# Performance work log

Measured on AMD Instinct MI355X. Metric: run time of the kernel, lower is better.

The kernel has to match this reference:

```python
import jax, jax.numpy as jnp
import numpy as np

MAX_DISP = 200


def conv2d(x, w, b):
    # x: [N,C,H,W], w: [O,I,3,3], stride 1, pad 1 == SAME
    y = jax.lax.conv_general_dilated(x, w, (1, 1), 'SAME',
                                     dimension_numbers=('NCHW', 'OIHW', 'NCHW'))
    return y + b[None, :, None, None]


def bn(x, g, b, m, v):
    # eval-mode BatchNorm2d with running stats (eps=1e-5)
    inv = jax.lax.rsqrt(v[None, :, None, None] + 1e-5)
    return g[None, :, None, None] * (x - m[None, :, None, None]) * inv + b[None, :, None, None]


def cost_volume(left, right, max_disp):
    # left, right: [c,h,w]. cost[d,y,x] = sum_c left[c,y,x] * padded[c,y,x+d]
    # where padded = [zeros(c,h,D), right] along w -- exact math of the torch loop.
    c, h, w = left.shape
    padded = jnp.concatenate([jnp.zeros((c, h, max_disp), left.dtype), right], axis=-1)

    def corr(d):
        win = jax.lax.dynamic_slice_in_dim(padded, d, w, axis=2)  # [c,h,w]
        return jnp.sum(left * win, axis=0)  # [h,w]

    return jax.vmap(corr)(jnp.arange(max_disp))  # [D,h,w]


def setup_inputs() -> dict:
    key = jax.random.key(0)
    ks = jax.random.split(key, 32)
    C, H, W = 32, 128, 256
    D = MAX_DISP
    inp = {}
    inp['left'] = jax.random.normal(ks[0], (1, C, H, W), jnp.float32)
    inp['right'] = jax.random.normal(ks[1], (1, C, H, W), jnp.float32)
    chans = [(64, D), (32, 64), (8, 32)]
    i = 2
    for idx, (co, ci) in enumerate(chans, 1):
        inp[f'w{idx}'] = jax.random.normal(ks[i], (co, ci, 3, 3), jnp.float32) * 0.05; i += 1
        inp[f'b{idx}'] = jax.random.normal(ks[i], (co,), jnp.float32) * 0.05; i += 1
        inp[f'g{idx}'] = 1.0 + 0.1 * jax.random.normal(ks[i], (co,), jnp.float32); i += 1
        inp[f'be{idx}'] = 0.1 * jax.random.normal(ks[i], (co,), jnp.float32); i += 1
        inp[f'm{idx}'] = 0.1 * jax.random.normal(ks[i], (co,), jnp.float32); i += 1
        inp[f'v{idx}'] = jax.random.uniform(ks[i], (co,), jnp.float32, minval=0.5, maxval=1.5); i += 1
    inp['w4'] = jax.random.normal(ks[i], (1, 8, 3, 3), jnp.float32) * 0.05; i += 1
    inp['b4'] = jax.random.normal(ks[i], (1,), jnp.float32) * 0.05
    return inp


def reference(left, right, w1, b1, g1, be1, m1, v1, w2, b2, g2, be2, m2, v2,
              w3, b3, g3, be3, m3, v3, w4, b4):
    vol = cost_volume(left[0], right[0], MAX_DISP)[None]  # [1, D, H, W]
    x = jax.nn.relu(bn(conv2d(vol, w1, b1), g1, be1, m1, v1))
    x = jax.nn.relu(bn(conv2d(x, w2, b2), g2, be2, m2, v2))
    x = jax.nn.relu(bn(conv2d(x, w3, b3), g3, be3, m3, v3))
    x = conv2d(x, w4, b4)
    return x[0]  # [1, H, W] (torch squeezes batch dim 0)
```

## Files before the change

### kernel.cpp

```cpp
#include <hip/hip_runtime.h>

#define HH 128
#define WW 256
#define CV_C 32
#define DISP 200

typedef __attribute__((ext_vector_type(4))) float f32x4;
typedef __attribute__((ext_vector_type(8))) short bf16x8;

__device__ inline unsigned short f2bf(float f) {
  unsigned int u = __float_as_uint(f);
  u = (u + 0x7FFFu + ((u >> 16) & 1u)) >> 16;
  return (unsigned short)u;
}

__device__ inline float bf2f(short s) {
  return __uint_as_float(((unsigned int)(unsigned short)s) << 16);
}

#define MAP_YX4()                                   \
  const int slot = bid >> 3;                        \
  const int y = ((bid & 7) << 4) + (slot & 15);     \
  const int x0 = (slot >> 4) << 6;

__global__ __launch_bounds__(256) void k1_cv_pack(
    const float* __restrict__ left, const float* __restrict__ right,
    const float* __restrict__ w1, const float* __restrict__ w2,
    const float* __restrict__ w3, unsigned short* __restrict__ pw1,
    unsigned short* __restrict__ pb2, unsigned short* __restrict__ pb3,
    unsigned short* __restrict__ cost_t) {
  __shared__ unsigned short r_sh[272][40];
  __shared__ unsigned short l_hi[64][40];
  __shared__ unsigned short l_lo[64][40];
  __shared__ unsigned short c_sh[64][224];
  const int bid = blockIdx.x;
  const int tid = threadIdx.x;

  if (bid >= 512) {
    const int b = bid - 512;
    if (b < 504) {
      const int idx = b * 256 + tid;
      const int j = idx & 7;
      const int n = (idx >> 3) & 63;
      const int kg = (idx >> 9) & 3;
      const int cp = idx >> 11;
      const int pos = cp % 9;
      const int chunk = cp / 9;
      const int ci = chunk * 32 + kg * 8 + j;
      float v = 0.f;
      if (ci < 200) v = w1[(n * 200 + ci) * 9 + pos];
      pw1[idx] = f2bf(v);
    } else if (b < 576) {
      const int idx = (b - 504) * 256 + tid;
      const int j = idx & 7;
      const int n = (idx >> 3) & 31;
      const int kg = (idx >> 8) & 3;
      const int kc = (idx >> 10) & 1;
      const int pos = idx >> 11;
      const int ci = kc * 32 + kg * 8 + j;
      pb2[idx] = f2bf(w2[(n * 64 + ci) * 9 + pos]);
    } else {
      const int idx = (b - 576) * 256 + tid;
      const int j = idx & 7;
      const int n = (idx >> 3) & 15;
      const int kg = (idx >> 7) & 3;
      const int pos = idx >> 9;
      const int ci = kg * 8 + j;
      float v = 0.f;
      if (n < 8) v = w3[(n * 32 + ci) * 9 + pos];
      pb3[idx] = f2bf(v);
    }
    return;
  }

  MAP_YX4();
  const int lane = tid & 63;
  const int wv = tid >> 6;
  const int col = lane & 15;
  const int kg = lane >> 4;

  for (int c = wv; c < CV_C; c += 4) {
    const float v = left[(c * HH + y) * WW + x0 + lane];
    const unsigned short h = f2bf(v);
    l_hi[lane][c] = h;
    l_lo[lane][c] = f2bf(v - bf2f(h));
  }
  for (int c = wv; c < CV_C; c += 4) {
    for (int pq = 0; pq < 320; pq += 64) {
      const int p = pq + lane;
      if (p < 272) {
        const int xp = x0 - 208 + p;
        float v = (xp >= 0) ? right[(c * HH + y) * WW + xp] : 0.f;
        r_sh[p][c] = f2bf(v);
      }
    }
  }
  {
    bf16x8 z = {0, 0, 0, 0, 0, 0, 0, 0};
    bf16x8* cz = (bf16x8*)c_sh;
#pragma unroll
    for (int k = 0; k < 7; ++k) cz[k * 256 + tid] = z;
  }
  __syncthreads();

  const bf16x8 b_hi = *(const bf16x8*)&l_hi[16 * wv + col][kg * 8];
  const bf16x8 b_lo = *(const bf16x8*)&l_lo[16 * wv + col][kg * 8];

  for (int t = 0; t < 14; ++t) {
    const int pq = 16 * (wv - t) + 208;
    const bf16x8 a_r = *(const bf16x8*)&r_sh[pq + col][kg * 8];
    f32x4 acc = {0.f, 0.f, 0.f, 0.f};
    acc = __builtin_amdgcn_mfma_f32_16x16x32_bf16(a_r, b_hi, acc, 0, 0, 0);
    acc = __builtin_amdgcn_mfma_f32_16x16x32_bf16(a_r, b_lo, acc, 0, 0, 0);
#pragma unroll
    for (int r = 0; r < 4; ++r) {
      const int d = 200 - 16 * t + kg * 4 + r - col;
      if (d >= 0 && d < DISP) c_sh[16 * wv + col][d] = f2bf(acc[r]);
    }
  }
  __syncthreads();

#pragma unroll
  for (int k = 0; k < 7; ++k) {
    const int s = k * 256 + tid;
    const int x = s / 28;
    const int dv = s - x * 28;
    *reinterpret_cast<bf16x8*>(&cost_t[(y * WW + x0 + x) * 224 + dv * 8]) =
        *reinterpret_cast<const bf16x8*>(&c_sh[x][dv * 8]);
  }
}

__global__ __launch_bounds__(256) void conv1_mfma_kernel(
    const unsigned short* __restrict__ cost_t,
    const unsigned short* __restrict__ pw,
    const float* __restrict__ bias, const float* __restrict__ gam,
    const float* __restrict__ bet, const float* __restrict__ mean,
    const float* __restrict__ var, unsigned short* __restrict__ out_t) {
  __shared__ unsigned short a_sh[4 * 66 * 40];
  __shared__ unsigned short b_sh[9 * 4 * 64 * 8];
  const int bid = blockIdx.x;
  const int tid = threadIdx.x;
  const int slot = bid >> 3;
  const int p = ((bid & 7) << 3) + (slot & 7);
  const int y0 = p << 1;
  const int x0 = (slot >> 3) << 6;
  const int lane = tid & 63;
  const int wv = tid >> 6;
  const int r = wv >> 1;
  const int n0 = (wv & 1) * 32;
  const int col = lane & 15;
  const int kg = lane >> 4;

  long goff[5];
  int laddr[5];
  bool gvalid[5], lvalid[5];
#pragma unroll
  for (int it = 0; it < 5; ++it) {
    const int i = tid + it * 256;
    lvalid[it] = i < 1056;
    const int row = i / 264;
    const int rem = i % 264;
    const int xx = rem >> 2;
    const int q = rem & 3;
    const int gy = y0 + row - 1;
    const int gx = x0 - 1 + xx;
    gvalid[it] = lvalid[it] && gy >= 0 && gy < HH && gx >= 0 && gx < WW;
    goff[it] = gvalid[it] ? (long)(gy * WW + gx) * 224 + q * 8 : 0;
    laddr[it] = (row * 66 + xx) * 40 + q * 8;
  }

  f32x4 acc[4][2];
#pragma unroll
  for (int i = 0; i < 4; ++i)
#pragma unroll
    for (int jx = 0; jx < 2; ++jx) acc[i][jx] = 0.f;

  const bf16x8* pwv = (const bf16x8*)pw;
  bf16x8* bsl = (bf16x8*)b_sh;
  const bf16x8 zero = {0, 0, 0, 0, 0, 0, 0, 0};
  bf16x8 stgA[5], stgB[9];

#pragma unroll
  for (int it = 0; it < 5; ++it)
    stgA[it] = gvalid[it] ? *reinterpret_cast<const bf16x8*>(&cost_t[goff[it]])
                          : zero;
#pragma unroll
  for (int it = 0; it < 9; ++it) stgB[it] = pwv[tid + it * 256];
#pragma unroll
  for (int it = 0; it < 5; ++it)
    if (lvalid[it]) *reinterpret_cast<bf16x8*>(&a_sh[laddr[it]]) = stgA[it];
#pragma unroll
  for (int it = 0; it < 9; ++it) bsl[tid + it * 256] = stgB[it];
  __syncthreads();

  for (int chunk = 0; chunk < 7; ++chunk) {
    if (chunk < 6) {
#pragma unroll
      for (int it = 0; it < 5; ++it)
        stgA[it] = gvalid[it] ? *reinterpret_cast<const bf16x8*>(
                                    &cost_t[goff[it] + (chunk + 1) * 32])
                              : zero;
      const bf16x8* pwn = pwv + (chunk + 1) * 2304;
#pragma unroll
      for (int it = 0; it < 9; ++it) stgB[it] = pwn[tid + it * 256];
    }
    const bf16x8* av = (const bf16x8*)a_sh;
#pragma unroll
    for (int pos = 0; pos < 9; ++pos) {
      const int ky = pos / 3;
      const int kx = pos % 3;
      const bf16x8 b0v = bsl[(pos * 4 + kg) * 64 + n0 + col];
      const bf16x8 b1v = bsl[(pos * 4 + kg) * 64 + n0 + 16 + col];
      bf16x8 af[4];
#pragma unroll
      for (int mt = 0; mt < 4; ++mt)
        af[mt] = av[((r + ky) * 66 + mt * 16 + col + kx) * 5 + kg];
#pragma unroll
      for (int mt = 0; mt < 4; ++mt) {
        acc[mt][0] =
            __builtin_amdgcn_mfma_f32_16x16x32_bf16(af[mt], b0v, acc[mt][0], 0, 0, 0);
        acc[mt][1] =
            __builtin_amdgcn_mfma_f32_16x16x32_bf16(af[mt], b1v, acc[mt][1], 0, 0, 0);
      }
    }
    if (chunk < 6) {
      __syncthreads();
#pragma unroll
      for (int it = 0; it < 5; ++it)
        if (lvalid[it]) *reinterpret_cast<bf16x8*>(&a_sh[laddr[it]]) = stgA[it];
#pragma unroll
      for (int it = 0; it < 9; ++it) bsl[tid + it * 256] = stgB[it];
      __syncthreads();
    }
  }

  const int y = y0 + r;
#pragma unroll
  for (int nf = 0; nf < 2; ++nf) {
    const int c = n0 + nf * 16 + col;
    const float inv = rsqrtf(var[c] + 1e-5f);
    const float sc = gam[c] * inv;
    const float sh = bet[c] - mean[c] * sc;
    const float bb = bias[c];
#pragma unroll
    for (int mt = 0; mt < 4; ++mt) {
#pragma unroll
      for (int rr = 0; rr < 4; ++rr) {
        const int m = mt * 16 + kg * 4 + rr;
        float vv = (acc[mt][nf][rr] + bb) * sc + sh;
        vv = fmaxf(vv, 0.f);
        out_t[((y * WW + x0 + m) << 6) + c] = f2bf(vv);
      }
    }
  }
}

__global__ __launch_bounds__(256) void conv2_mfma_kernel(
    const unsigned short* __restrict__ in_t,
    const unsigned short* __restrict__ pb,
    const float* __restrict__ bias, const float* __restrict__ gam,
    const float* __restrict__ bet, const float* __restrict__ mean,
    const float* __restrict__ var, unsigned short* __restrict__ out_t) {
  __shared__ unsigned short a_sh[3 * 66 * 64];
  __shared__ unsigned short b_sh[18432];
  char* const ab = (char*)a_sh;
  const int bid = blockIdx.x;
  const int tid = threadIdx.x;
  MAP_YX4();
  const int lane = tid & 63;
  const int wv = tid >> 6;
  const int m0 = (wv >> 1) * 32;
  const int n0 = (wv & 1) * 16;
  const int col = lane & 15;
  const int kg = lane >> 4;

  f32x4 acc[2];
  acc[0] = 0.f;
  acc[1] = 0.f;

  {
    const bf16x8* pbv = (const bf16x8*)pb;
    bf16x8* bsl = (bf16x8*)b_sh;
#pragma unroll
    for (int it = 0; it < 9; ++it) bsl[tid + it * 256] = pbv[tid + it * 256];
  }
  for (int i = tid; i < 1584; i += 256) {
    const int r = i >> 3;
    const int q = i & 7;
    const int rowy = r / 66;
    const int xx = r % 66;
    const int gy = y + rowy - 1;
    const int gx = x0 - 1 + xx;
    bf16x8 v = {0, 0, 0, 0, 0, 0, 0, 0};
    if (gy >= 0 && gy < HH && gx >= 0 && gx < WW)
      v = *reinterpret_cast<const bf16x8*>(&in_t[((gy * WW + gx) << 6) + q * 8]);
    const int byte = ((r << 7) + (q << 4)) ^ ((r & 7) << 4);
    *reinterpret_cast<bf16x8*>(ab + byte) = v;
  }
  __syncthreads();

  const bf16x8* bsl = (const bf16x8*)b_sh;
#pragma unroll
  for (int pos = 0; pos < 9; ++pos) {
    const int ky = pos / 3;
    const int kx = pos % 3;
#pragma unroll
    for (int kc = 0; kc < 2; ++kc) {
      const bf16x8 bv = bsl[((pos * 2 + kc) * 4 + kg) * 32 + n0 + col];
#pragma unroll
      for (int mf = 0; mf < 2; ++mf) {
        const int r = ky * 66 + m0 + mf * 16 + col + kx;
        const int byte = ((r << 7) + (kc << 6) + (kg << 4)) ^ ((r & 7) << 4);
        const bf16x8 av = *reinterpret_cast<const bf16x8*>(ab + byte);
        acc[mf] = __builtin_amdgcn_mfma_f32_16x16x32_bf16(av, bv, acc[mf], 0, 0, 0);
      }
    }
  }

  const int c = n0 + col;
  const float inv = rsqrtf(var[c] + 1e-5f);
  const float sc = gam[c] * inv;
  const float sh = bet[c] - mean[c] * sc;
  const float bb = bias[c];
#pragma unroll
  for (int mf = 0; mf < 2; ++mf) {
#pragma unroll
    for (int rr = 0; rr < 4; ++rr) {
      const int m = m0 + mf * 16 + kg * 4 + rr;
      float vv = (acc[mf][rr] + bb) * sc + sh;
      vv = fmaxf(vv, 0.f);
      out_t[((y * WW + x0 + m) << 5) + c] = f2bf(vv);
    }
  }
}

__global__ __launch_bounds__(256) void conv3_mfma_kernel(
    const unsigned short* __restrict__ in_t,
    const unsigned short* __restrict__ pb,
    const float* __restrict__ bias, const float* __restrict__ gam,
    const float* __restrict__ bet, const float* __restrict__ mean,
    const float* __restrict__ var, unsigned short* __restrict__ out_t) {
  __shared__ unsigned short a_sh[3 * 66 * 32];
  __shared__ unsigned short b_sh[4608];
  char* const ab = (char*)a_sh;
  const int bid = blockIdx.x;
  const int tid = threadIdx.x;
  MAP_YX4();
  const int lane = tid & 63;
  const int wv = tid >> 6;
  const int m0 = wv * 16;
  const int col = lane & 15;
  const int kg = lane >> 4;

  f32x4 acc = 0.f;

  {
    const bf16x8* pbv = (const bf16x8*)pb;
    bf16x8* bsl = (bf16x8*)b_sh;
    for (int s = tid; s < 576; s += 256) bsl[s] = pbv[s];
  }
  for (int i = tid; i < 792; i += 256) {
    const int r = i >> 2;
    const int q = i & 3;
    const int rowy = r / 66;
    const int xx = r % 66;
    const int gy = y + rowy - 1;
    const int gx = x0 - 1 + xx;
    bf16x8 v = {0, 0, 0, 0, 0, 0, 0, 0};
    if (gy >= 0 && gy < HH && gx >= 0 && gx < WW)
      v = *reinterpret_cast<const bf16x8*>(&in_t[((gy * WW + gx) << 5) + q * 8]);
    const int byte = ((r << 6) + (q << 4)) ^ ((r & 3) << 4);
    *reinterpret_cast<bf16x8*>(ab + byte) = v;
  }
  __syncthreads();

  const bf16x8* bsl = (const bf16x8*)b_sh;
#pragma unroll
  for (int pos = 0; pos < 9; ++pos) {
    const int ky = pos / 3;
    const int kx = pos % 3;
    const bf16x8 bv = bsl[(pos * 4 + kg) * 16 + col];
    const int r = ky * 66 + m0 + col + kx;
    const int byte = ((r << 6) + (kg << 4)) ^ ((r & 3) << 4);
    const bf16x8 av = *reinterpret_cast<const bf16x8*>(ab + byte);
    acc = __builtin_amdgcn_mfma_f32_16x16x32_bf16(av, bv, acc, 0, 0, 0);
  }

  if (col < 8) {
    const int c = col;
    const float inv = rsqrtf(var[c] + 1e-5f);
    const float sc = gam[c] * inv;
    const float sh = bet[c] - mean[c] * sc;
    const float bb = bias[c];
#pragma unroll
    for (int rr = 0; rr < 4; ++rr) {
      const int m = m0 + kg * 4 + rr;
      float vv = (acc[rr] + bb) * sc + sh;
      vv = fmaxf(vv, 0.f);
      out_t[((y * WW + x0 + m) << 3) + c] = f2bf(vv);
    }
  }
}

__global__ __launch_bounds__(256) void conv4_kernel(
    const unsigned short* __restrict__ in_t, const float* __restrict__ w4,
    const float* __restrict__ b4, float* __restrict__ out) {
  const int bid = blockIdx.x;
  const int y = ((bid & 7) << 4) + (bid >> 3);
  const int x = threadIdx.x;

  float wr[3][3][8];
#pragma unroll
  for (int ci = 0; ci < 8; ++ci)
#pragma unroll
    for (int ky = 0; ky < 3; ++ky)
#pragma unroll
      for (int kx = 0; kx < 3; ++kx) wr[ky][kx][ci] = w4[(ci * 3 + ky) * 3 + kx];

  float acc = b4[0];
#pragma unroll
  for (int ky = 0; ky < 3; ++ky) {
    const int gy = y + ky - 1;
    if (gy < 0 || gy >= HH) continue;
#pragma unroll
    for (int kx = 0; kx < 3; ++kx) {
      const int gx = x + kx - 1;
      if (gx < 0 || gx >= WW) continue;
      const bf16x8 v =
          *reinterpret_cast<const bf16x8*>(&in_t[((gy << 8) + gx) << 3]);
#pragma unroll
      for (int ci = 0; ci < 8; ++ci) acc += bf2f(v[ci]) * wr[ky][kx][ci];
    }
  }
  out[y * WW + x] = acc;
}

extern "C" void kernel_launch(void* const* d_in, const int* in_sizes, int n_in,
                              void* d_out, int out_size, void* d_ws,
                              size_t ws_size, hipStream_t stream) {
  const float* left = (const float*)d_in[0];
  const float* right = (const float*)d_in[1];
  const float* w1 = (const float*)d_in[2];
  const float* b1 = (const float*)d_in[3];
  const float* g1 = (const float*)d_in[4];
  const float* be1 = (const float*)d_in[5];
  const float* m1 = (const float*)d_in[6];
  const float* v1 = (const float*)d_in[7];
  const float* w2 = (const float*)d_in[8];
  const float* b2 = (const float*)d_in[9];
  const float* g2 = (const float*)d_in[10];
  const float* be2 = (const float*)d_in[11];
  const float* m2 = (const float*)d_in[12];
  const float* v2 = (const float*)d_in[13];
  const float* w3 = (const float*)d_in[14];
  const float* b3 = (const float*)d_in[15];
  const float* g3 = (const float*)d_in[16];
  const float* be3 = (const float*)d_in[17];
  const float* m3 = (const float*)d_in[18];
  const float* v3 = (const float*)d_in[19];
  const float* w4 = (const float*)d_in[20];
  const float* b4 = (const float*)d_in[21];

  char* ws = (char*)d_ws;
  unsigned short* cost_t = (unsigned short*)ws;
  char* region = ws + 14680064;
  unsigned short* pw1 = (unsigned short*)(region + 0);
  unsigned short* pb2 = (unsigned short*)(region + 262144);
  unsigned short* pb3 = (unsigned short*)(region + 327680);
  unsigned short* o1t = (unsigned short*)(region + 393216);
  unsigned short* o2t = (unsigned short*)(region + 4587520);
  unsigned short* o3t = (unsigned short*)(region + 6684672);
  float* o4 = (float*)d_out;

  k1_cv_pack<<<1106, 256, 0, stream>>>(left, right, w1, w2, w3, pw1, pb2, pb3,
                                       cost_t);
  conv1_mfma_kernel<<<256, 256, 0, stream>>>(cost_t, pw1, b1, g1, be1, m1, v1,
                                             o1t);
  conv2_mfma_kernel<<<512, 256, 0, stream>>>(o1t, pb2, b2, g2, be2, m2, v2,
                                             o2t);
  conv3_mfma_kernel<<<512, 256, 0, stream>>>(o2t, pb3, b3, g3, be3, m3, v3,
                                             o3t);
  conv4_kernel<<<128, 256, 0, stream>>>(o3t, w4, b4, o4);
}
```

Baseline: 48.88 us.

## Fuse conv3 and conv4 into one kernel with halo recompute in LDS

```diff
diff --git a/kernel.cpp b/kernel.cpp
--- a/kernel.cpp
+++ b/kernel.cpp
@@ -334,38 +334,41 @@
   }
 }
 
-__global__ __launch_bounds__(256) void conv3_mfma_kernel(
+__global__ __launch_bounds__(256) void conv34_fused_kernel(
     const unsigned short* __restrict__ in_t,
     const unsigned short* __restrict__ pb,
     const float* __restrict__ bias, const float* __restrict__ gam,
     const float* __restrict__ bet, const float* __restrict__ mean,
-    const float* __restrict__ var, unsigned short* __restrict__ out_t) {
-  __shared__ unsigned short a_sh[3 * 66 * 32];
+    const float* __restrict__ var, const float* __restrict__ w4,
+    const float* __restrict__ b4, float* __restrict__ out) {
+  __shared__ unsigned short o2s[5 * 84 * 32];
   __shared__ unsigned short b_sh[4608];
-  char* const ab = (char*)a_sh;
+  __shared__ unsigned short o3s[3 * 80 * 8];
+  char* const ab = (char*)o2s;
   const int bid = blockIdx.x;
   const int tid = threadIdx.x;
   MAP_YX4();
   const int lane = tid & 63;
   const int wv = tid >> 6;
-  const int m0 = wv * 16;
   const int col = lane & 15;
   const int kg = lane >> 4;
-
-  f32x4 acc = 0.f;
 
   {
     const bf16x8* pbv = (const bf16x8*)pb;
     bf16x8* bsl = (bf16x8*)b_sh;
     for (int s = tid; s < 576; s += 256) bsl[s] = pbv[s];
   }
-  for (int i = tid; i < 792; i += 256) {
+  if (tid < 240) {
+    bf16x8 z = {0, 0, 0, 0, 0, 0, 0, 0};
+    ((bf16x8*)o3s)[tid] = z;
+  }
+  for (int i = tid; i < 1680; i += 256) {
     const int r = i >> 2;
     const int q = i & 3;
-    const int rowy = r / 66;
-    const int xx = r % 66;
-    const int gy = y + rowy - 1;
-    const int gx = x0 - 1 + xx;
+    const int rowy = r / 84;
+    const int xx = r % 84;
+    const int gy = y - 2 + rowy;
+    const int gx = x0 - 2 + xx;
     bf16x8 v = {0, 0, 0, 0, 0, 0, 0, 0};
     if (gy >= 0 && gy < HH && gx >= 0 && gx < WW)
       v = *reinterpret_cast<const bf16x8*>(&in_t[((gy * WW + gx) << 5) + q * 8]);
@@ -375,64 +378,65 @@
   __syncthreads();
 
   const bf16x8* bsl = (const bf16x8*)b_sh;
-#pragma unroll
-  for (int pos = 0; pos < 9; ++pos) {
-    const int ky = pos / 3;
-    const int kx = pos % 3;
-    const bf16x8 bv = bsl[(pos * 4 + kg) * 16 + col];
-    const int r = ky * 66 + m0 + col + kx;
-    const int byte = ((r << 6) + (kg << 4)) ^ ((r & 3) << 4);
-    const bf16x8 av = *reinterpret_cast<const bf16x8*>(ab + byte);
-    acc = __builtin_amdgcn_mfma_f32_16x16x32_bf16(av, bv, acc, 0, 0, 0);
-  }
-
-  if (col < 8) {
-    const int c = col;
-    const float inv = rsqrtf(var[c] + 1e-5f);
-    const float sc = gam[c] * inv;
-    const float sh = bet[c] - mean[c] * sc;
-    const float bb = bias[c];
-#pragma unroll
-    for (int rr = 0; rr < 4; ++rr) {
-      const int m = m0 + kg * 4 + rr;
-      float vv = (acc[rr] + bb) * sc + sh;
-      vv = fmaxf(vv, 0.f);
-      out_t[((y * WW + x0 + m) << 3) + c] = f2bf(vv);
-    }
-  }
-}
-
-__global__ __launch_bounds__(256) void conv4_kernel(
-    const unsigned short* __restrict__ in_t, const float* __restrict__ w4,
-    const float* __restrict__ b4, float* __restrict__ out) {
-  const int bid = blockIdx.x;
-  const int y = ((bid & 7) << 4) + (bid >> 3);
-  const int x = threadIdx.x;
-
-  float wr[3][3][8];
-#pragma unroll
-  for (int ci = 0; ci < 8; ++ci)
-#pragma unroll
-    for (int ky = 0; ky < 3; ++ky)
-#pragma unroll
-      for (int kx = 0; kx < 3; ++kx) wr[ky][kx][ci] = w4[(ci * 3 + ky) * 3 + kx];
-
-  float acc = b4[0];
-#pragma unroll
-  for (int ky = 0; ky < 3; ++ky) {
-    const int gy = y + ky - 1;
-    if (gy < 0 || gy >= HH) continue;
-#pragma unroll
-    for (int kx = 0; kx < 3; ++kx) {
-      const int gx = x + kx - 1;
-      if (gx < 0 || gx >= WW) continue;
-      const bf16x8 v =
-          *reinterpret_cast<const bf16x8*>(&in_t[((gy << 8) + gx) << 3]);
-#pragma unroll
-      for (int ci = 0; ci < 8; ++ci) acc += bf2f(v[ci]) * wr[ky][kx][ci];
-    }
-  }
-  out[y * WW + x] = acc;
+  const int c3 = col < 8 ? col : 7;
+  const float inv3 = rsqrtf(var[c3] + 1e-5f);
+  const float sc3 = gam[c3] * inv3;
+  const float sh3 = bet[c3] - mean[c3] * sc3;
+  const float bb3 = bias[c3];
+
+  for (int jb = wv; jb < 15; jb += 4) {
+    const int ry = jb / 5;
+    const int xt = jb % 5;
+    f32x4 acc = {0.f, 0.f, 0.f, 0.f};
+#pragma unroll
+    for (int pos = 0; pos < 9; ++pos) {
+      const int ky = pos / 3;
+      const int kx = pos % 3;
+      const bf16x8 bv = bsl[(pos * 4 + kg) * 16 + col];
+      const int r = (ry + ky) * 84 + 16 * xt + col + kx;
+      const int byte = ((r << 6) + (kg << 4)) ^ ((r & 3) << 4);
+      const bf16x8 av = *reinterpret_cast<const bf16x8*>(ab + byte);
+      acc = __builtin_amdgcn_mfma_f32_16x16x32_bf16(av, bv, acc, 0, 0, 0);
+    }
+    if (col < 8) {
+      const int gyo = y - 1 + ry;
+#pragma unroll
+      for (int rr = 0; rr < 4; ++rr) {
+        const int pxl = 16 * xt + kg * 4 + rr;
+        const int gxo = x0 - 1 + pxl;
+        if (gyo >= 0 && gyo < HH && gxo >= 0 && gxo < WW) {
+          float vv = (acc[rr] + bb3) * sc3 + sh3;
+          vv = fmaxf(vv, 0.f);
+          o3s[(ry * 80 + pxl) * 8 + col] = f2bf(vv);
+        }
+      }
+    }
+  }
+  __syncthreads();
+
+  if (tid < 64) {
+    const int x = x0 + tid;
+    float wr[3][3][8];
+#pragma unroll
+    for (int ci = 0; ci < 8; ++ci)
+#pragma unroll
+      for (int ky = 0; ky < 3; ++ky)
+#pragma unroll
+        for (int kx = 0; kx < 3; ++kx)
+          wr[ky][kx][ci] = w4[(ci * 3 + ky) * 3 + kx];
+    float acc = b4[0];
+    const bf16x8* o3v = (const bf16x8*)o3s;
+#pragma unroll
+    for (int ky = 0; ky < 3; ++ky) {
+#pragma unroll
+      for (int kx = 0; kx < 3; ++kx) {
+        const bf16x8 v = o3v[ky * 80 + tid + kx];
+#pragma unroll
+        for (int ci = 0; ci < 8; ++ci) acc += bf2f(v[ci]) * wr[ky][kx][ci];
+      }
+    }
+    out[y * WW + x] = acc;
+  }
 }
 
 extern "C" void kernel_launch(void* const* d_in, const int* in_sizes, int n_in,
@@ -469,7 +473,6 @@
   unsigned short* pb3 = (unsigned short*)(region + 327680);
   unsigned short* o1t = (unsigned short*)(region + 393216);
   unsigned short* o2t = (unsigned short*)(region + 4587520);
-  unsigned short* o3t = (unsigned short*)(region + 6684672);
   float* o4 = (float*)d_out;
 
   k1_cv_pack<<<1106, 256, 0, stream>>>(left, right, w1, w2, w3, pw1, pb2, pb3,
@@ -478,7 +481,6 @@
                                              o1t);
   conv2_mfma_kernel<<<512, 256, 0, stream>>>(o1t, pb2, b2, g2, be2, m2, v2,
                                              o2t);
-  conv3_mfma_kernel<<<512, 256, 0, stream>>>(o2t, pb3, b3, g3, be3, m3, v3,
-                                             o3t);
-  conv4_kernel<<<128, 256, 0, stream>>>(o3t, w4, b4, o4);
-}
+  conv34_fused_kernel<<<512, 256, 0, stream>>>(o2t, pb3, b3, g3, be3, m3, v3,
+                                               w4, b4, o4);
+}
```

Result: no change. 48.24 us (-1.3%).
